# Kernel optimization log

Measured on AMD Instinct MI355X. Metric: run time of the kernel, lower is better.

Reference implementation:

```python
import jax, jax.numpy as jnp
import numpy as np

N_NODES = 100000
N_EDGES = 1200000
IN_CH, HID_CH, OUT_CH = 64, 64, 32


def setup_inputs() -> dict:
    key = jax.random.key(0)
    ks = jax.random.split(key, 8)
    x = jax.random.normal(ks[0], (N_NODES, IN_CH), dtype=jnp.float32)
    edge_index = jax.random.randint(ks[1], (2, N_EDGES), 0, N_NODES, dtype=jnp.int64)
    # SAGEConv params: lin_l acts on aggregated neighbors (has bias), lin_r on root features.
    def glorot(k, fan_in, fan_out):
        s = jnp.sqrt(6.0 / (fan_in + fan_out))
        return jax.random.uniform(k, (fan_in, fan_out), jnp.float32, -s, s)
    W1_l = glorot(ks[2], IN_CH, HID_CH)
    W1_r = glorot(ks[3], IN_CH, HID_CH)
    b1 = jnp.zeros((HID_CH,), jnp.float32)
    W2_l = glorot(ks[4], HID_CH, OUT_CH)
    W2_r = glorot(ks[5], HID_CH, OUT_CH)
    b2 = jnp.zeros((OUT_CH,), jnp.float32)
    return {"x": x, "edge_index": edge_index, "W1_l": W1_l, "W1_r": W1_r,
            "b1": b1, "W2_l": W2_l, "W2_r": W2_r, "b2": b2}


def _sage_conv(h, src, dst, W_l, W_r, b):
    # gather source-node features along edges, mean-aggregate at destinations
    msg = h[src]                                               # [E, d]
    agg = jax.ops.segment_sum(msg, dst, num_segments=N_NODES)  # [N, d]
    cnt = jax.ops.segment_sum(jnp.ones((msg.shape[0],), h.dtype), dst,
                              num_segments=N_NODES)
    agg = agg / jnp.maximum(cnt, 1.0)[:, None]                 # mean (0 if no neighbors)
    return agg @ W_l + h @ W_r + b


def reference(x, edge_index, W1_l, W1_r, b1, W2_l, W2_r, b2):
    src, dst = edge_index[0], edge_index[1]
    h = _sage_conv(x, src, dst, W1_l, W1_r, b1)
    h = jax.nn.relu(h)
    # dropout is identity in eval mode
    return _sage_conv(h, src, dst, W2_l, W2_r, b2)
```

## Files before the change

kernel.cpp:

```cpp
#include <hip/hip_runtime.h>

__device__ __forceinline__ float bf2f(unsigned short u) {
    union { unsigned int i; float f; } v;
    v.i = ((unsigned int)u) << 16;
    return v.f;
}
__device__ __forceinline__ unsigned short f2bf(float f) {
    union { float f; unsigned int u; } v;
    v.f = f;
    unsigned int u = v.u;
    u += 0x7FFFu + ((u >> 16) & 1u);
    return (unsigned short)(u >> 16);
}
__device__ __forceinline__ float loadElem(const void* p, size_t i, int isb) {
    return isb ? bf2f(((const unsigned short*)p)[i]) : ((const float*)p)[i];
}
__device__ __forceinline__ void fma4(float4& a, float s, const float4& w) {
    a.x += s * w.x; a.y += s * w.y; a.z += s * w.z; a.w += s * w.w;
}
__device__ __forceinline__ float bflo(unsigned int u) {
    union { unsigned int i; float f; } v; v.i = u << 16; return v.f;
}
__device__ __forceinline__ float bfhi(unsigned int u) {
    union { unsigned int i; float f; } v; v.i = u & 0xFFFF0000u; return v.f;
}

#define CHUNK 4096
#define BSHIFT 8

__global__ void k_detect(const int* __restrict__ ei, int newords,
                         const unsigned int* __restrict__ xw, int nxw,
                         int* __restrict__ flags) {
    __shared__ int aOr;
    __shared__ int plaus;
    if (threadIdx.x == 0) { aOr = 0; plaus = 0; }
    __syncthreads();
    int v = 0;
    for (int i = 1 + 2 * (int)threadIdx.x; i < newords; i += 512) v |= ei[i];
    int pl = 0;
    for (int i = threadIdx.x; i < nxw; i += 256) {
        unsigned short lo = (unsigned short)(xw[i] & 0xFFFFu);
        float a = fabsf(bf2f(lo));
        if (a > 1e-5f && a < 100.0f) pl++;
    }
    atomicOr(&aOr, v);
    atomicAdd(&plaus, pl);
    __syncthreads();
    if (threadIdx.x == 0) {
        flags[0] = (aOr == 0) ? 1 : 0;
        flags[1] = (2 * plaus >= nxw) ? 1 : 0;
    }
}

__global__ void k_cast(const void* __restrict__ x, unsigned short* __restrict__ xb,
                       int n8, const int* __restrict__ flags) {
    int i = blockIdx.x * blockDim.x + threadIdx.x;
    if (i >= n8) return;
    if (flags[1]) {
        ((uint4*)xb)[i] = ((const uint4*)x)[i];
    } else {
        const float4* xf = (const float4*)x;
        float4 a = xf[2 * i], b = xf[2 * i + 1];
        ushort4 lo = { f2bf(a.x), f2bf(a.y), f2bf(a.z), f2bf(a.w) };
        ushort4 hi = { f2bf(b.x), f2bf(b.y), f2bf(b.z), f2bf(b.w) };
        ((ushort4*)xb)[2 * i] = lo;
        ((ushort4*)xb)[2 * i + 1] = hi;
    }
}

__global__ __launch_bounds__(256) void k_bcount(
        const int* __restrict__ ei, const int* __restrict__ flags,
        int* __restrict__ blockHist, int E, int NBUK, int nblk) {
    __shared__ int hist[512];
    int t = threadIdx.x;
    for (int i = t; i < NBUK; i += 256) hist[i] = 0;
    __syncthreads();
    int q = flags[0];
    int e0 = blockIdx.x * CHUNK, e1 = min(E, e0 + CHUNK);
    for (int e = e0 + t; e < e1; e += 256) {
        int dst = ei[((size_t)(E + e)) << q];
        atomicAdd(&hist[dst >> BSHIFT], 1);
    }
    __syncthreads();
    for (int i = t; i < NBUK; i += 256)
        blockHist[(size_t)i * nblk + blockIdx.x] = hist[i];
}

__global__ __launch_bounds__(256) void k_rowscan(
        int* __restrict__ blockHist, int* __restrict__ bukTot, int nblk) {
    __shared__ int sh[256];
    int t = threadIdx.x;
    int* row = blockHist + (size_t)blockIdx.x * nblk;
    int carry = 0;
    for (int base = 0; base < nblk; base += 256) {
        int i = base + t;
        int v = (i < nblk) ? row[i] : 0;
        sh[t] = v;
        __syncthreads();
        for (int off = 1; off < 256; off <<= 1) {
            int u = (t >= off) ? sh[t - off] : 0;
            __syncthreads();
            sh[t] += u;
            __syncthreads();
        }
        if (i < nblk) row[i] = carry + sh[t] - v;
        int tot = sh[255];
        __syncthreads();
        carry += tot;
    }
    if (t == 0) bukTot[blockIdx.x] = carry;
}

__global__ __launch_bounds__(512) void k_toto(
        const int* __restrict__ bukTot, int* __restrict__ bukOff,
        int* __restrict__ rowptr, int NBUK, int E, int N) {
    __shared__ int sh[512];
    int t = threadIdx.x;
    int v = (t < NBUK) ? bukTot[t] : 0;
    sh[t] = v;
    __syncthreads();
    for (int off = 1; off < 512; off <<= 1) {
        int u = (t >= off) ? sh[t - off] : 0;
        __syncthreads();
        sh[t] += u;
        __syncthreads();
    }
    if (t < NBUK) bukOff[t] = sh[t] - v;
    if (t == 0) { bukOff[NBUK] = E; rowptr[N] = E; }
}

__global__ __launch_bounds__(256) void k_part(
        const int* __restrict__ ei, const int* __restrict__ flags,
        const int* __restrict__ blockHist, const int* __restrict__ bukOff,
        unsigned int* __restrict__ recs, int E, int NBUK, int nblk) {
    __shared__ int cur[512];
    int t = threadIdx.x;
    for (int i = t; i < NBUK; i += 256)
        cur[i] = blockHist[(size_t)i * nblk + blockIdx.x] + bukOff[i];
    __syncthreads();
    int q = flags[0];
    int e0 = blockIdx.x * CHUNK, e1 = min(E, e0 + CHUNK);
    for (int e = e0 + t; e < e1; e += 256) {
        int dst = ei[((size_t)(E + e)) << q];
        int src = ei[((size_t)e) << q];
        int pos = atomicAdd(&cur[dst >> BSHIFT], 1);
        recs[pos] = ((unsigned int)src << BSHIFT) | (unsigned int)(dst & ((1 << BSHIFT) - 1));
    }
}

__global__ __launch_bounds__(256) void k_csr(
        const unsigned int* __restrict__ recs, const int* __restrict__ bukOff,
        int* __restrict__ rowptr, int* __restrict__ esorted, int N) {
    __shared__ int degLoc[256];
    __shared__ int offLoc[256];
    __shared__ int wcur[256];
    int t = threadIdx.x;
    int node0 = blockIdx.x << BSHIFT;
    int r0 = bukOff[blockIdx.x], r1 = bukOff[blockIdx.x + 1];
    degLoc[t] = 0;
    __syncthreads();
    for (int i = r0 + t; i < r1; i += 256)
        atomicAdd(&degLoc[recs[i] & 255], 1);
    __syncthreads();
    int v = degLoc[t];
    offLoc[t] = v;
    __syncthreads();
    for (int off = 1; off < 256; off <<= 1) {
        int u = (t >= off) ? offLoc[t - off] : 0;
        __syncthreads();
        offLoc[t] += u;
        __syncthreads();
    }
    int excl = offLoc[t] - v;
    int node = node0 + t;
    if (node < N) rowptr[node] = r0 + excl;
    wcur[t] = r0 + excl;
    __syncthreads();
    for (int i = r0 + t; i < r1; i += 256) {
        unsigned int rec = recs[i];
        int pos = atomicAdd(&wcur[rec & 255], 1);
        esorted[pos] = (int)(rec >> BSHIFT);
    }
}

template<int CHOUT, bool RELU, bool FINAL>
__global__ __launch_bounds__(256) void k_fused(
        const unsigned short* __restrict__ feat,
        const int* __restrict__ rowptr,
        const int* __restrict__ esorted,
        const void* __restrict__ Wl,
        const void* __restrict__ Wr,
        const void* __restrict__ bias,
        void* __restrict__ outp,
        int N, const int* __restrict__ flags) {
    constexpr int SA = 68;
    __shared__ float amBuf[64 * SA];
    __shared__ unsigned short wS16[64 * CHOUT];
    __shared__ float Bs[CHOUT];

    int t = threadIdx.x;
    int isb = flags[1];
    int node0 = blockIdx.x << 6;

    if (isb) {
        for (int i = t; i < (64 * CHOUT) / 8; i += 256)
            ((uint4*)wS16)[i] = ((const uint4*)Wl)[i];
    } else {
        for (int i = t; i < 64 * CHOUT; i += 256)
            wS16[i] = f2bf(((const float*)Wl)[i]);
    }
    if (t < CHOUT) Bs[t] = loadElem(bias, t, isb);

    {
        int g = t >> 4, l = t & 15;
        int gb = (t & 63) & ~15;
#pragma unroll
        for (int jj = 0; jj < 4; ++jj) {
            int nl = g + 16 * jj;
            int node = node0 + nl;
            float ax = 0.f, ay = 0.f, az = 0.f, aw = 0.f;
            float inv = 0.f;
            if (node < N) {
                int beg = rowptr[node], end = rowptr[node + 1];
                int d = end - beg;
                if (d > 0) {
                    inv = 1.0f / (float)d;
                    for (int bs = beg; bs < end; bs += 16) {
                        int cnt = min(end - bs, 16);
                        int idx = esorted[min(bs + l, end - 1)];
                        int dd = 0;
                        for (; dd + 4 <= cnt; dd += 4) {
                            int s0 = __shfl(idx, gb + dd + 0, 64);
                            int s1 = __shfl(idx, gb + dd + 1, 64);
                            int s2 = __shfl(idx, gb + dd + 2, 64);
                            int s3 = __shfl(idx, gb + dd + 3, 64);
                            ushort4 u0 = *(const ushort4*)(feat + (size_t)s0 * 64 + 4 * l);
                            ushort4 u1 = *(const ushort4*)(feat + (size_t)s1 * 64 + 4 * l);
                            ushort4 u2 = *(const ushort4*)(feat + (size_t)s2 * 64 + 4 * l);
                            ushort4 u3 = *(const ushort4*)(feat + (size_t)s3 * 64 + 4 * l);
                            ax += bf2f(u0.x) + bf2f(u1.x) + bf2f(u2.x) + bf2f(u3.x);
                            ay += bf2f(u0.y) + bf2f(u1.y) + bf2f(u2.y) + bf2f(u3.y);
                            az += bf2f(u0.z) + bf2f(u1.z) + bf2f(u2.z) + bf2f(u3.z);
                            aw += bf2f(u0.w) + bf2f(u1.w) + bf2f(u2.w) + bf2f(u3.w);
                        }
                        for (; dd < cnt; ++dd) {
                            int s = __shfl(idx, gb + dd, 64);
                            ushort4 u = *(const ushort4*)(feat + (size_t)s * 64 + 4 * l);
                            ax += bf2f(u.x); ay += bf2f(u.y);
                            az += bf2f(u.z); aw += bf2f(u.w);
                        }
                    }
                }
            }
            *(float4*)&amBuf[nl * SA + 4 * l] =
                make_float4(ax * inv, ay * inv, az * inv, aw * inv);
        }
    }
    __syncthreads();

    constexpr int CQ = CHOUT / 4;
    constexpr int NPT = CHOUT / 16;
    int cq = t % CQ, nq = t / CQ;
    float4 acc[NPT];
#pragma unroll
    for (int j = 0; j < NPT; ++j) acc[j] = make_float4(0.f, 0.f, 0.f, 0.f);

#pragma unroll 8
    for (int k = 0; k < 64; ++k) {
        uint2 wu = *(const uint2*)&wS16[k * CHOUT + 4 * cq];
        float4 w = make_float4(bflo(wu.x), bfhi(wu.x), bflo(wu.y), bfhi(wu.y));
#pragma unroll
        for (int j = 0; j < NPT; ++j)
            fma4(acc[j], amBuf[(nq * NPT + j) * SA + k], w);
    }
    __syncthreads();

    for (int i = t; i < 64 * 8; i += 256) {
        int nl = i >> 3, k0 = (i & 7) << 3;
        int gn = node0 + nl;
        float v[8];
        if (gn < N) {
            uint4 u = *(const uint4*)(feat + (size_t)gn * 64 + k0);
            v[0] = bflo(u.x); v[1] = bfhi(u.x);
            v[2] = bflo(u.y); v[3] = bfhi(u.y);
            v[4] = bflo(u.z); v[5] = bfhi(u.z);
            v[6] = bflo(u.w); v[7] = bfhi(u.w);
        } else {
#pragma unroll
            for (int j = 0; j < 8; ++j) v[j] = 0.f;
        }
#pragma unroll
        for (int j = 0; j < 8; ++j) amBuf[nl * SA + k0 + j] = v[j];
    }
    if (isb) {
        for (int i = t; i < (64 * CHOUT) / 8; i += 256)
            ((uint4*)wS16)[i] = ((const uint4*)Wr)[i];
    } else {
        for (int i = t; i < 64 * CHOUT; i += 256)
            wS16[i] = f2bf(((const float*)Wr)[i]);
    }
    __syncthreads();

#pragma unroll 8
    for (int k = 0; k < 64; ++k) {
        uint2 wu = *(const uint2*)&wS16[k * CHOUT + 4 * cq];
        float4 w = make_float4(bflo(wu.x), bfhi(wu.x), bflo(wu.y), bfhi(wu.y));
#pragma unroll
        for (int j = 0; j < NPT; ++j)
            fma4(acc[j], amBuf[(nq * NPT + j) * SA + k], w);
    }

    float4 bv = *(const float4*)&Bs[4 * cq];
#pragma unroll
    for (int j = 0; j < NPT; ++j) {
        int nl = nq * NPT + j;
        int node = node0 + nl;
        if (node >= N) continue;
        float4 r = acc[j];
        r.x += bv.x; r.y += bv.y; r.z += bv.z; r.w += bv.w;
        if (RELU) {
            r.x = fmaxf(r.x, 0.f); r.y = fmaxf(r.y, 0.f);
            r.z = fmaxf(r.z, 0.f); r.w = fmaxf(r.w, 0.f);
        }
        if (FINAL && !isb) {
            *(float4*)((float*)outp + (size_t)node * CHOUT + 4 * cq) = r;
        } else {
            ushort4 o = { f2bf(r.x), f2bf(r.y), f2bf(r.z), f2bf(r.w) };
            *(ushort4*)((unsigned short*)outp + (size_t)node * CHOUT + 4 * cq) = o;
        }
    }
}

extern "C" void kernel_launch(void* const* d_in, const int* in_sizes, int n_in,
                              void* d_out, int out_size, void* d_ws, size_t ws_size,
                              hipStream_t stream) {
    const void* x   = d_in[0];
    const int*  ei  = (const int*)d_in[1];
    const void* W1l = d_in[2];
    const void* W1r = d_in[3];
    const void* b1  = d_in[4];
    const void* W2l = d_in[5];
    const void* W2r = d_in[6];
    const void* b2  = d_in[7];

    const int N = in_sizes[0] / 64;
    const int E = in_sizes[1] / 2;
    const int NBUK = (N + (1 << BSHIFT) - 1) >> BSHIFT;
    const int nblk = (E + CHUNK - 1) / CHUNK;

    char* base = (char*)d_ws;
    size_t off = 0;
    auto alloc = [&](size_t bytes) { size_t o = off; off = (off + bytes + 255) & ~(size_t)255; return o; };
    int* flags   = (int*)(base + alloc(256));
    int* bukTot  = (int*)(base + alloc((size_t)NBUK * 4));
    int* bukOff  = (int*)(base + alloc((size_t)(NBUK + 1) * 4));
    int* rowptr  = (int*)(base + alloc((size_t)(N + 1) * 4));
    unsigned int* recs = (unsigned int*)(base + alloc((size_t)E * 4));
    int* esorted = (int*)(base + alloc((size_t)E * 4));
    unsigned short* xb = (unsigned short*)(base + alloc((size_t)N * 64 * 2));
    unsigned short* h  = (unsigned short*)(base + alloc((size_t)N * 64 * 2));
    (void)ws_size;

    int* blockHist = (int*)xb;

    const int B = 256;
    int nd = 2 * E; if (nd > 2048) nd = 2048;

    k_detect<<<1, 256, 0, stream>>>(ei, nd, (const unsigned int*)x, 512, flags);
    k_bcount<<<nblk, B, 0, stream>>>(ei, flags, blockHist, E, NBUK, nblk);
    k_rowscan<<<NBUK, B, 0, stream>>>(blockHist, bukTot, nblk);
    k_toto<<<1, 512, 0, stream>>>(bukTot, bukOff, rowptr, NBUK, E, N);
    k_part<<<nblk, B, 0, stream>>>(ei, flags, blockHist, bukOff, recs, E, NBUK, nblk);
    k_cast<<<(N * 8 + B - 1) / B, B, 0, stream>>>(x, xb, N * 8, flags);
    k_csr<<<NBUK, B, 0, stream>>>(recs, bukOff, rowptr, esorted, N);

    const int ntile = (N + 63) / 64;
    k_fused<64, true, false><<<ntile, B, 0, stream>>>(xb, rowptr, esorted,
                                                      W1l, W1r, b1, h, N, flags);
    k_fused<32, false, true><<<ntile, B, 0, stream>>>(h, rowptr, esorted,
                                                      W2l, W2r, b2, d_out, N, flags);
}
```

Baseline: 236.9 us.

## Project layer-2 features before aggregation and shrink CSR bucket sizes

Layer 2 now first multiplies h by W2_l in a separate GEMM kernel producing 32-wide bf16 rows. A new fused kernel then mean-aggregates those narrower rows and adds h@W2_r plus bias. This halves the per-edge gather width in the second layer, at the cost of an extra kernel launch and an intermediate write/read plus one more bf16 rounding. The CSR build also uses smaller chunks and 128-node buckets, with a multi-pass bucket-offset scan.

New measurement: 251.1 us. +6.0%, slower.

```diff
diff --git a/kernel.cpp b/kernel.cpp
--- a/kernel.cpp
+++ b/kernel.cpp
@@ -25,8 +25,9 @@
     union { unsigned int i; float f; } v; v.i = u & 0xFFFF0000u; return v.f;
 }
 
-#define CHUNK 4096
-#define BSHIFT 8
+#define CHUNK 1024
+#define BSHIFT 7
+#define BN (1 << BSHIFT)
 
 __global__ void k_detect(const int* __restrict__ ei, int newords,
                          const unsigned int* __restrict__ xw, int nxw,
@@ -71,7 +72,7 @@
 __global__ __launch_bounds__(256) void k_bcount(
         const int* __restrict__ ei, const int* __restrict__ flags,
         int* __restrict__ blockHist, int E, int NBUK, int nblk) {
-    __shared__ int hist[512];
+    __shared__ int hist[1024];
     int t = threadIdx.x;
     for (int i = t; i < NBUK; i += 256) hist[i] = 0;
     __syncthreads();
@@ -111,21 +112,28 @@
     if (t == 0) bukTot[blockIdx.x] = carry;
 }
 
-__global__ __launch_bounds__(512) void k_toto(
+__global__ __launch_bounds__(1024) void k_toto(
         const int* __restrict__ bukTot, int* __restrict__ bukOff,
         int* __restrict__ rowptr, int NBUK, int E, int N) {
-    __shared__ int sh[512];
-    int t = threadIdx.x;
-    int v = (t < NBUK) ? bukTot[t] : 0;
-    sh[t] = v;
-    __syncthreads();
-    for (int off = 1; off < 512; off <<= 1) {
-        int u = (t >= off) ? sh[t - off] : 0;
+    __shared__ int sh[1024];
+    int t = threadIdx.x;
+    int carry = 0;
+    for (int base = 0; base < NBUK; base += 1024) {
+        int i = base + t;
+        int v = (i < NBUK) ? bukTot[i] : 0;
+        sh[t] = v;
         __syncthreads();
-        sh[t] += u;
+        for (int off = 1; off < 1024; off <<= 1) {
+            int u = (t >= off) ? sh[t - off] : 0;
+            __syncthreads();
+            sh[t] += u;
+            __syncthreads();
+        }
+        if (i < NBUK) bukOff[i] = carry + sh[t] - v;
+        int tot = sh[1023];
         __syncthreads();
-    }
-    if (t < NBUK) bukOff[t] = sh[t] - v;
+        carry += tot;
+    }
     if (t == 0) { bukOff[NBUK] = E; rowptr[N] = E; }
 }
 
@@ -133,7 +141,7 @@
         const int* __restrict__ ei, const int* __restrict__ flags,
         const int* __restrict__ blockHist, const int* __restrict__ bukOff,
         unsigned int* __restrict__ recs, int E, int NBUK, int nblk) {
-    __shared__ int cur[512];
+    __shared__ int cur[1024];
     int t = threadIdx.x;
     for (int i = t; i < NBUK; i += 256)
         cur[i] = blockHist[(size_t)i * nblk + blockIdx.x] + bukOff[i];
@@ -144,41 +152,43 @@
         int dst = ei[((size_t)(E + e)) << q];
         int src = ei[((size_t)e) << q];
         int pos = atomicAdd(&cur[dst >> BSHIFT], 1);
-        recs[pos] = ((unsigned int)src << BSHIFT) | (unsigned int)(dst & ((1 << BSHIFT) - 1));
+        recs[pos] = ((unsigned int)src << BSHIFT) | (unsigned int)(dst & (BN - 1));
     }
 }
 
 __global__ __launch_bounds__(256) void k_csr(
         const unsigned int* __restrict__ recs, const int* __restrict__ bukOff,
         int* __restrict__ rowptr, int* __restrict__ esorted, int N) {
-    __shared__ int degLoc[256];
-    __shared__ int offLoc[256];
-    __shared__ int wcur[256];
+    __shared__ int degLoc[BN];
+    __shared__ int offLoc[BN];
+    __shared__ int wcur[BN];
     int t = threadIdx.x;
     int node0 = blockIdx.x << BSHIFT;
     int r0 = bukOff[blockIdx.x], r1 = bukOff[blockIdx.x + 1];
-    degLoc[t] = 0;
+    if (t < BN) degLoc[t] = 0;
     __syncthreads();
     for (int i = r0 + t; i < r1; i += 256)
-        atomicAdd(&degLoc[recs[i] & 255], 1);
-    __syncthreads();
-    int v = degLoc[t];
-    offLoc[t] = v;
-    __syncthreads();
-    for (int off = 1; off < 256; off <<= 1) {
-        int u = (t >= off) ? offLoc[t - off] : 0;
+        atomicAdd(&degLoc[recs[i] & (BN - 1)], 1);
+    __syncthreads();
+    int v = (t < BN) ? degLoc[t] : 0;
+    if (t < BN) offLoc[t] = v;
+    __syncthreads();
+    for (int off = 1; off < BN; off <<= 1) {
+        int u = (t >= off && t < BN) ? offLoc[t - off] : 0;
         __syncthreads();
-        offLoc[t] += u;
+        if (t < BN) offLoc[t] += u;
         __syncthreads();
     }
-    int excl = offLoc[t] - v;
-    int node = node0 + t;
-    if (node < N) rowptr[node] = r0 + excl;
-    wcur[t] = r0 + excl;
+    if (t < BN) {
+        int excl = offLoc[t] - v;
+        int node = node0 + t;
+        if (node < N) rowptr[node] = r0 + excl;
+        wcur[t] = r0 + excl;
+    }
     __syncthreads();
     for (int i = r0 + t; i < r1; i += 256) {
         unsigned int rec = recs[i];
-        int pos = atomicAdd(&wcur[rec & 255], 1);
+        int pos = atomicAdd(&wcur[rec & (BN - 1)], 1);
         esorted[pos] = (int)(rec >> BSHIFT);
     }
 }
@@ -331,6 +341,189 @@
     }
 }
 
+__global__ __launch_bounds__(256) void k_gemm32(
+        const unsigned short* __restrict__ A,
+        const void* __restrict__ W,
+        unsigned short* __restrict__ D,
+        int N, const int* __restrict__ flags) {
+    constexpr int S = 130;
+    __shared__ float As[64 * S];
+    __shared__ unsigned short wS16[64 * 32];
+
+    int t = threadIdx.x;
+    int isb = flags[1];
+    if (isb) {
+        for (int i = t; i < (64 * 32) / 8; i += 256)
+            ((uint4*)wS16)[i] = ((const uint4*)W)[i];
+    } else {
+        for (int i = t; i < 64 * 32; i += 256)
+            wS16[i] = f2bf(((const float*)W)[i]);
+    }
+    int nodeBase = blockIdx.x * 128;
+    for (int i = t; i < 128 * 8; i += 256) {
+        int node = i >> 3, k0 = (i & 7) << 3;
+        int gn = nodeBase + node;
+        float v[8];
+        if (gn < N) {
+            uint4 u = *(const uint4*)(A + (size_t)gn * 64 + k0);
+            v[0] = bflo(u.x); v[1] = bfhi(u.x);
+            v[2] = bflo(u.y); v[3] = bfhi(u.y);
+            v[4] = bflo(u.z); v[5] = bfhi(u.z);
+            v[6] = bflo(u.w); v[7] = bfhi(u.w);
+        } else {
+#pragma unroll
+            for (int j = 0; j < 8; ++j) v[j] = 0.f;
+        }
+#pragma unroll
+        for (int j = 0; j < 8; ++j) As[(k0 + j) * S + node] = v[j];
+    }
+    __syncthreads();
+
+    int cq = t % 8, nq = t / 8;
+    float4 acc[4];
+    acc[0] = acc[1] = acc[2] = acc[3] = make_float4(0.f, 0.f, 0.f, 0.f);
+
+#pragma unroll 8
+    for (int k = 0; k < 64; ++k) {
+        uint2 wu = *(const uint2*)&wS16[k * 32 + 4 * cq];
+        float4 w = make_float4(bflo(wu.x), bfhi(wu.x), bflo(wu.y), bfhi(wu.y));
+        const float* ar = &As[k * S + 4 * nq];
+        float2 a01 = *(const float2*)ar;
+        float2 a23 = *(const float2*)(ar + 2);
+        fma4(acc[0], a01.x, w);
+        fma4(acc[1], a01.y, w);
+        fma4(acc[2], a23.x, w);
+        fma4(acc[3], a23.y, w);
+    }
+
+#pragma unroll
+    for (int i = 0; i < 4; ++i) {
+        int node = nodeBase + 4 * nq + i;
+        if (node >= N) continue;
+        float4 r = acc[i];
+        ushort4 o = { f2bf(r.x), f2bf(r.y), f2bf(r.z), f2bf(r.w) };
+        *(ushort4*)(D + (size_t)node * 32 + 4 * cq) = o;
+    }
+}
+
+__global__ __launch_bounds__(256) void k_fused2(
+        const unsigned short* __restrict__ y2,
+        const unsigned short* __restrict__ h,
+        const int* __restrict__ rowptr,
+        const int* __restrict__ esorted,
+        const void* __restrict__ Wr,
+        const void* __restrict__ bias,
+        void* __restrict__ outp,
+        int N, const int* __restrict__ flags) {
+    constexpr int SAM = 36;
+    constexpr int SH = 68;
+    __shared__ float amB[64 * SAM];
+    __shared__ unsigned short hS16[64 * SH];
+    __shared__ unsigned short wS16[64 * 32];
+    __shared__ float Bs[32];
+
+    int t = threadIdx.x;
+    int isb = flags[1];
+    int node0 = blockIdx.x << 6;
+
+    if (isb) {
+        for (int i = t; i < (64 * 32) / 8; i += 256)
+            ((uint4*)wS16)[i] = ((const uint4*)Wr)[i];
+    } else {
+        for (int i = t; i < 64 * 32; i += 256)
+            wS16[i] = f2bf(((const float*)Wr)[i]);
+    }
+    if (t < 32) Bs[t] = loadElem(bias, t, isb);
+
+    for (int i = t; i < 64 * 8; i += 256) {
+        int nl = i >> 3, k0 = (i & 7) << 3;
+        int gn = node0 + nl;
+        uint4 u = make_uint4(0, 0, 0, 0);
+        if (gn < N) u = *(const uint4*)(h + (size_t)gn * 64 + k0);
+        *(uint2*)&hS16[nl * SH + k0]     = make_uint2(u.x, u.y);
+        *(uint2*)&hS16[nl * SH + k0 + 4] = make_uint2(u.z, u.w);
+    }
+
+    {
+        int g = t >> 3, l = t & 7;
+        int gb = (t & 63) & ~7;
+#pragma unroll
+        for (int jj = 0; jj < 2; ++jj) {
+            int nl = g + 32 * jj;
+            int node = node0 + nl;
+            float ax = 0.f, ay = 0.f, az = 0.f, aw = 0.f;
+            float inv = 0.f;
+            if (node < N) {
+                int beg = rowptr[node], end = rowptr[node + 1];
+                int d = end - beg;
+                if (d > 0) {
+                    inv = 1.0f / (float)d;
+                    for (int bs = beg; bs < end; bs += 8) {
+                        int cnt = min(end - bs, 8);
+                        int idx = esorted[min(bs + l, end - 1)];
+                        int dd = 0;
+                        for (; dd + 4 <= cnt; dd += 4) {
+                            int s0 = __shfl(idx, gb + dd + 0, 64);
+                            int s1 = __shfl(idx, gb + dd + 1, 64);
+                            int s2 = __shfl(idx, gb + dd + 2, 64);
+                            int s3 = __shfl(idx, gb + dd + 3, 64);
+                            ushort4 u0 = *(const ushort4*)(y2 + (size_t)s0 * 32 + 4 * l);
+                            ushort4 u1 = *(const ushort4*)(y2 + (size_t)s1 * 32 + 4 * l);
+                            ushort4 u2 = *(const ushort4*)(y2 + (size_t)s2 * 32 + 4 * l);
+                            ushort4 u3 = *(const ushort4*)(y2 + (size_t)s3 * 32 + 4 * l);
+                            ax += bf2f(u0.x) + bf2f(u1.x) + bf2f(u2.x) + bf2f(u3.x);
+                            ay += bf2f(u0.y) + bf2f(u1.y) + bf2f(u2.y) + bf2f(u3.y);
+                            az += bf2f(u0.z) + bf2f(u1.z) + bf2f(u2.z) + bf2f(u3.z);
+                            aw += bf2f(u0.w) + bf2f(u1.w) + bf2f(u2.w) + bf2f(u3.w);
+                        }
+                        for (; dd < cnt; ++dd) {
+                            int s = __shfl(idx, gb + dd, 64);
+                            ushort4 u = *(const ushort4*)(y2 + (size_t)s * 32 + 4 * l);
+                            ax += bf2f(u.x); ay += bf2f(u.y);
+                            az += bf2f(u.z); aw += bf2f(u.w);
+                        }
+                    }
+                }
+            }
+            *(float4*)&amB[nl * SAM + 4 * l] =
+                make_float4(ax * inv, ay * inv, az * inv, aw * inv);
+        }
+    }
+    __syncthreads();
+
+    int cq = t % 8, nq = t / 8;
+    float4 acc0 = make_float4(0.f, 0.f, 0.f, 0.f);
+    float4 acc1 = make_float4(0.f, 0.f, 0.f, 0.f);
+
+#pragma unroll 8
+    for (int k = 0; k < 64; ++k) {
+        uint2 wu = *(const uint2*)&wS16[k * 32 + 4 * cq];
+        float4 w = make_float4(bflo(wu.x), bfhi(wu.x), bflo(wu.y), bfhi(wu.y));
+        float a0 = bf2f(hS16[(2 * nq) * SH + k]);
+        float a1 = bf2f(hS16[(2 * nq + 1) * SH + k]);
+        fma4(acc0, a0, w);
+        fma4(acc1, a1, w);
+    }
+
+    float4 bv = *(const float4*)&Bs[4 * cq];
+#pragma unroll
+    for (int j = 0; j < 2; ++j) {
+        int nl = 2 * nq + j;
+        int node = node0 + nl;
+        if (node >= N) continue;
+        float4 r = (j == 0) ? acc0 : acc1;
+        float4 ap = *(const float4*)&amB[nl * SAM + 4 * cq];
+        r.x += ap.x + bv.x; r.y += ap.y + bv.y;
+        r.z += ap.z + bv.z; r.w += ap.w + bv.w;
+        if (!isb) {
+            *(float4*)((float*)outp + (size_t)node * 32 + 4 * cq) = r;
+        } else {
+            ushort4 o = { f2bf(r.x), f2bf(r.y), f2bf(r.z), f2bf(r.w) };
+            *(ushort4*)((unsigned short*)outp + (size_t)node * 32 + 4 * cq) = o;
+        }
+    }
+}
+
 extern "C" void kernel_launch(void* const* d_in, const int* in_sizes, int n_in,
                               void* d_out, int out_size, void* d_ws, size_t ws_size,
                               hipStream_t stream) {
@@ -345,7 +538,7 @@
 
     const int N = in_sizes[0] / 64;
     const int E = in_sizes[1] / 2;
-    const int NBUK = (N + (1 << BSHIFT) - 1) >> BSHIFT;
+    const int NBUK = (N + BN - 1) >> BSHIFT;
     const int nblk = (E + CHUNK - 1) / CHUNK;
 
     char* base = (char*)d_ws;
@@ -362,6 +555,7 @@
     (void)ws_size;
 
     int* blockHist = (int*)xb;
+    unsigned short* y2 = xb;
 
     const int B = 256;
     int nd = 2 * E; if (nd > 2048) nd = 2048;
@@ -369,7 +563,7 @@
     k_detect<<<1, 256, 0, stream>>>(ei, nd, (const unsigned int*)x, 512, flags);
     k_bcount<<<nblk, B, 0, stream>>>(ei, flags, blockHist, E, NBUK, nblk);
     k_rowscan<<<NBUK, B, 0, stream>>>(blockHist, bukTot, nblk);
-    k_toto<<<1, 512, 0, stream>>>(bukTot, bukOff, rowptr, NBUK, E, N);
+    k_toto<<<1, 1024, 0, stream>>>(bukTot, bukOff, rowptr, NBUK, E, N);
     k_part<<<nblk, B, 0, stream>>>(ei, flags, blockHist, bukOff, recs, E, NBUK, nblk);
     k_cast<<<(N * 8 + B - 1) / B, B, 0, stream>>>(x, xb, N * 8, flags);
     k_csr<<<NBUK, B, 0, stream>>>(recs, bukOff, rowptr, esorted, N);
@@ -377,6 +571,7 @@
     const int ntile = (N + 63) / 64;
     k_fused<64, true, false><<<ntile, B, 0, stream>>>(xb, rowptr, esorted,
                                                       W1l, W1r, b1, h, N, flags);
-    k_fused<32, false, true><<<ntile, B, 0, stream>>>(h, rowptr, esorted,
-                                                      W2l, W2r, b2, d_out, N, flags);
-}
+    k_gemm32<<<(N + 127) / 128, B, 0, stream>>>(h, W2l, y2, N, flags);
+    k_fused2<<<ntile, B, 0, stream>>>(y2, h, rowptr, esorted, W2r, b2,
+                                      d_out, N, flags);
+}
```
